# Performance work log

Hardware: AMD Instinct MI355X
Metric: run time of the kernel (lower is better)

## Reference

```python
import jax, jax.numpy as jnp
import numpy as np

B, N, D = 32, 2048, 128
HALF = D // 2
DT = 0.01  # interval = [0.0, 0.01], euler solver -> single step of size 0.01


def setup_inputs() -> dict:
    key = jax.random.key(0)
    ks = jax.random.split(key, 10)
    x = jax.random.normal(ks[0], (B, N, D), dtype=jnp.float32)
    hz = jax.random.normal(ks[1], (B, N, D), dtype=jnp.float32)
    # row-normalized random adjacency so adj @ h stays O(1) (avoids tanh saturation)
    adj = jax.random.uniform(ks[2], (N, N), dtype=jnp.float32) / N
    W1 = jax.random.normal(ks[3], (D, D), dtype=jnp.float32) * 0.05
    W2 = jax.random.normal(ks[4], (D, D), dtype=jnp.float32) * 0.05
    Wa = jax.random.normal(ks[5], (2 * D, 2 * D), dtype=jnp.float32) * 0.05
    ba = jnp.zeros((2 * D,), dtype=jnp.float32)
    Wb = jax.random.normal(ks[6], (2 * D, D), dtype=jnp.float32) * 0.05
    bb = jnp.zeros((D,), dtype=jnp.float32)
    # nn.Parameter init is zeros in torch; randomize in [0,0.1] for a nontrivial baseline
    eps = jax.random.uniform(ks[7], (B, N, HALF), dtype=jnp.float32) * 0.1
    return {"x": x, "hz": hz, "adj": adj, "W1": W1, "W2": W2,
            "Wa": Wa, "ba": ba, "Wb": Wb, "bb": bb, "eps": eps}


def reference(x, hz, adj, W1, W2, Wa, ba, Wb, bb, eps):
    # MLP gating: Linear(2D,2D) -> ReLU -> Linear(2D,D) -> Tanh
    u = jnp.concatenate([x, hz], axis=-1)            # [B,N,2D]
    h = jnp.tanh(jax.nn.relu(u @ Wa + ba) @ Wb + bb)  # [B,N,D]

    def gnn_func(h, W):
        # f(t, h) = tanh(A @ h @ W)  (graph diffusion ODE func)
        return jnp.tanh(jnp.einsum('nm,bmd->bnd', adj, h) @ W)

    def euler_step(h, W):
        # odeint(euler, t=[0, 0.01]): one step y1 = y0 + dt * f(0, y0)
        return h + DT * gnn_func(h, W)

    eps_c = jnp.clip(eps, 0.0, 0.1)
    for _ in range(2):
        h_f = euler_step(h, W1)[..., :HALF]                      # [B,N,D/2]
        h = jnp.concatenate([h_f, h[..., HALF:]], axis=-1)       # [B,N,D]
        h_s = eps_c * euler_step(h, W2)[..., HALF:]              # [B,N,D/2]
        h = jnp.concatenate([h_f, h_s], axis=-1)                 # [B,N,D]
    return h
```

## Files before the change

kernel.cpp:

```cpp
#include <hip/hip_runtime.h>


typedef unsigned short u16;
typedef unsigned int   u32;
typedef unsigned long long u64;
typedef __attribute__((ext_vector_type(8))) short bf8;
typedef __attribute__((ext_vector_type(4))) float f4;

#define AS1 __attribute__((address_space(1)))
#define AS3 __attribute__((address_space(3)))

__device__ __forceinline__ void gl_lds16(const void* g, void* l) {
  __builtin_amdgcn_global_load_lds((const AS1 u32*)g, (AS3 u32*)l, 16, 0, 0);
}
__device__ __forceinline__ float bf2f(u16 v) {
  u32 u = ((u32)v) << 16; return __builtin_bit_cast(float, u);
}
__device__ __forceinline__ u16 f2bf(float f) {
  u32 u = __builtin_bit_cast(u32, f);
  return (u16)((u + 0x7fffu + ((u >> 16) & 1u)) >> 16);
}
__device__ __forceinline__ float ldf(const void* p, size_t i, u32 isf32) {
  return isf32 ? ((const float*)p)[i] : bf2f(((const u16*)p)[i]);
}

__device__ __forceinline__ void stage128x32(const u16* grow0, int stride, u16* lds,
                                            int wave, int lane) {
  int r0 = wave * 16 + (lane >> 2);
  int c0 = (lane & 3) * 8;
  gl_lds16(grow0 + (size_t)r0 * stride + c0, lds + wave * 512);
  gl_lds16(grow0 + (size_t)(64 + r0) * stride + c0, lds + 2048 + wave * 512);
}
__device__ __forceinline__ void stage64x32(const u16* grow0, int stride, u16* lds,
                                           int wave, int lane) {
  gl_lds16(grow0 + (size_t)(wave * 16 + (lane >> 2)) * stride + (lane & 3) * 8,
           lds + wave * 512);
}

__global__ void detect_dtype(const u16* __restrict__ x_raw, u32* __restrict__ flag) {
  __shared__ int s;
  int tid = threadIdx.x;
  if (tid == 0) s = 0;
  __syncthreads();
  int huge = 0;
#pragma unroll
  for (int j = 0; j < 16; ++j) {
    u16 v = x_raw[tid * 16 + j];
    u32 e = (v >> 7) & 0xFF;
    if (e >= 0xC0) huge = 1;
  }
  if (huge) atomicOr(&s, 1);
  __syncthreads();
  if (tid == 0) flag[0] = (u32)s;
}

__global__ void cvt_bf16(const void* __restrict__ in, u16* __restrict__ out,
                         long in_off, int n, const u32* __restrict__ flag) {
  u32 isf32 = flag[0];
  int gid = blockIdx.x * 256 + threadIdx.x;
  long i = in_off + (long)gid * 4;
  if (gid * 4 >= n) return;
  u16 o0, o1, o2, o3;
  if (isf32) {
    f4 v = *(const f4*)&((const float*)in)[i];
    o0 = f2bf(v[0]); o1 = f2bf(v[1]); o2 = f2bf(v[2]); o3 = f2bf(v[3]);
  } else {
    u64 v = *(const u64*)&((const u16*)in)[i];
    o0 = (u16)v; o1 = (u16)(v >> 16); o2 = (u16)(v >> 32); o3 = (u16)(v >> 48);
  }
  u64 pk = (u64)o0 | ((u64)o1 << 16) | ((u64)o2 << 32) | ((u64)o3 << 48);
  *(u64*)&out[(size_t)gid * 4] = pk;
}

__global__ void prep_weights(const void* __restrict__ Wa, const void* __restrict__ Wb,
                             const void* __restrict__ W1, const void* __restrict__ W2,
                             u16* __restrict__ WaT, u16* __restrict__ WbT,
                             u16* __restrict__ W1T, u16* __restrict__ W2T,
                             const u32* __restrict__ flag) {
  u32 isf32 = flag[0];
  int i = blockIdx.x * 256 + threadIdx.x;
  if (i < 65536) {
    int o = i >> 8, k = i & 255; WaT[o * 256 + k] = f2bf(ldf(Wa, (size_t)k * 256 + o, isf32));
  } else if (i < 98304) {
    int j = i - 65536; int o = j >> 8, k = j & 255;
    WbT[o * 256 + k] = f2bf(ldf(Wb, (size_t)k * 128 + o, isf32));
  } else if (i < 106496) {
    int j = i - 98304; int jj = j >> 7, k = j & 127;
    W1T[jj * 128 + k] = f2bf(ldf(W1, (size_t)k * 128 + jj, isf32));
  } else {
    int j = i - 106496; int jj = j >> 7, k = j & 127;
    W2T[jj * 128 + k] = f2bf(ldf(W2, (size_t)k * 128 + 64 + jj, isf32));
  }
}

__global__ __launch_bounds__(256, 2) void mlp_fused(const void* __restrict__ x,
                                                    const void* __restrict__ hz,
                                                    const u16* __restrict__ WaT,
                                                    const void* __restrict__ ba,
                                                    const u16* __restrict__ WbT,
                                                    const void* __restrict__ bb,
                                                    const u16* __restrict__ W1T,
                                                    u16* __restrict__ hT,
                                                    u16* __restrict__ hW,
                                                    const u32* __restrict__ flag) {
  __shared__ __align__(16) u16 Z[64 * 264];
  __shared__ __align__(16) u16 pool[10240];
  u16* lA = pool;
  u16* lB = pool + 2048;
  u16* hN = pool;
  u32 isf32 = flag[0];
  int tid = threadIdx.x, lane = tid & 63, wave = tid >> 6;
  int col = lane & 15, quad = lane >> 4;
  int r0 = blockIdx.x * 64;
  int b = r0 >> 11;

  f4 acc[4][4] = {};
  for (int kk = 0; kk < 8; ++kk) {
    int k0 = kk * 32;
    const void* src = (kk < 4) ? x : hz;
    int csrc = (kk < 4) ? k0 : (k0 - 128);
    __syncthreads();
    {
      int row = tid >> 2, c0 = (tid & 3) * 8;
      size_t g = (size_t)(r0 + row) * 128 + csrc + c0;
      uint4 pk;
      if (isf32) {
        f4 v0 = *(const f4*)&((const float*)src)[g];
        f4 v1 = *(const f4*)&((const float*)src)[g + 4];
        pk.x = (u32)f2bf(v0[0]) | ((u32)f2bf(v0[1]) << 16);
        pk.y = (u32)f2bf(v0[2]) | ((u32)f2bf(v0[3]) << 16);
        pk.z = (u32)f2bf(v1[0]) | ((u32)f2bf(v1[1]) << 16);
        pk.w = (u32)f2bf(v1[2]) | ((u32)f2bf(v1[3]) << 16);
      } else {
        pk = *(const uint4*)&((const u16*)src)[g];
      }
      *(uint4*)&lA[row * 32 + c0] = pk;
    }
    stage128x32(WaT + k0, 256, lB, wave, lane);
    stage128x32(WaT + (size_t)128 * 256 + k0, 256, lB + 4096, wave, lane);
    __syncthreads();
    bf8 af[4], bfr[4];
#pragma unroll
    for (int mi = 0; mi < 4; ++mi) af[mi] = *(const bf8*)&lA[(mi * 16 + col) * 32 + quad * 8];
#pragma unroll
    for (int nj = 0; nj < 4; ++nj) bfr[nj] = *(const bf8*)&lB[(wave * 64 + nj * 16 + col) * 32 + quad * 8];
#pragma unroll
    for (int mi = 0; mi < 4; ++mi)
#pragma unroll
      for (int nj = 0; nj < 4; ++nj)
        acc[mi][nj] = __builtin_amdgcn_mfma_f32_16x16x32_bf16(af[mi], bfr[nj], acc[mi][nj], 0, 0, 0);
  }
#pragma unroll
  for (int mi = 0; mi < 4; ++mi)
#pragma unroll
    for (int nj = 0; nj < 4; ++nj) {
      int o = wave * 64 + nj * 16 + col;
      float bav = ldf(ba, o, isf32);
      int rl = mi * 16 + quad * 4;
#pragma unroll
      for (int r = 0; r < 4; ++r)
        Z[(rl + r) * 264 + o] = f2bf(fmaxf(acc[mi][nj][r] + bav, 0.f));
    }
  __syncthreads();

  f4 acc2[4][2] = {};
  for (int kk = 0; kk < 8; ++kk) {
    int k0 = kk * 32;
    if (kk) __syncthreads();
    stage128x32(WbT + k0, 256, lB, wave, lane);
    __syncthreads();
    bf8 az[4], bw[2];
#pragma unroll
    for (int mi = 0; mi < 4; ++mi) az[mi] = *(const bf8*)&Z[(mi * 16 + col) * 264 + k0 + quad * 8];
#pragma unroll
    for (int nj = 0; nj < 2; ++nj) bw[nj] = *(const bf8*)&lB[(wave * 32 + nj * 16 + col) * 32 + quad * 8];
#pragma unroll
    for (int mi = 0; mi < 4; ++mi)
#pragma unroll
      for (int nj = 0; nj < 2; ++nj)
        acc2[mi][nj] = __builtin_amdgcn_mfma_f32_16x16x32_bf16(az[mi], bw[nj], acc2[mi][nj], 0, 0, 0);
  }
  __syncthreads();

#pragma unroll
  for (int mi = 0; mi < 4; ++mi)
#pragma unroll
    for (int nj = 0; nj < 2; ++nj) {
      int d = wave * 32 + nj * 16 + col;
      float bbv = ldf(bb, d, isf32);
      int rl = mi * 16 + quad * 4;
      int rabs = r0 + rl;
      int n = rabs & 2047;
      u16 p[4];
#pragma unroll
      for (int r = 0; r < 4; ++r) {
        p[r] = f2bf(tanhf(acc2[mi][nj][r] + bbv));
        hN[(rl + r) * 136 + d] = p[r];
      }
      u64 pk = (u64)p[0] | ((u64)p[1] << 16) | ((u64)p[2] << 32) | ((u64)p[3] << 48);
      *(u64*)&hT[(size_t)(b * 128 + d) * 2048 + n] = pk;
    }
  __syncthreads();

  f4 acc3[4] = {};
#pragma unroll
  for (int ks = 0; ks < 4; ++ks) {
    bf8 aw[4], bg;
#pragma unroll
    for (int mi = 0; mi < 4; ++mi)
      aw[mi] = *(const bf8*)&W1T[(size_t)(mi * 16 + col) * 128 + ks * 32 + quad * 8];
    bg = *(const bf8*)&hN[(wave * 16 + col) * 136 + ks * 32 + quad * 8];
#pragma unroll
    for (int mi = 0; mi < 4; ++mi)
      acc3[mi] = __builtin_amdgcn_mfma_f32_16x16x32_bf16(aw[mi], bg, acc3[mi], 0, 0, 0);
  }
#pragma unroll
  for (int mi = 0; mi < 4; ++mi) {
    int rloc = wave * 16 + col;
    int ng = (r0 & 2047) + rloc;
#pragma unroll
    for (int r = 0; r < 4; ++r) {
      int j = mi * 16 + quad * 4 + r;
      hW[(size_t)(b * 64 + j) * 2048 + ng] = f2bf(acc3[mi][r]);
    }
  }
}

__global__ __launch_bounds__(256, 2) void fused_step2(const u16* __restrict__ hin,
                                                      const u16* __restrict__ hWT,
                                                      const u16* __restrict__ adjb,
                                                      const u16* __restrict__ WnT,
                                                      const void* __restrict__ eps,
                                                      u16* __restrict__ hout,
                                                      u16* __restrict__ hWout,
                                                      int half, const u32* __restrict__ flag) {
  __shared__ __align__(16) u16 smem[24576];
  u16* lA = smem;
  u16* lB = smem + 8192;
  u16* gN = smem;
  u32 isf32 = flag[0];
  int tid = threadIdx.x, lane = tid & 63, wave = tid >> 6;
  int col = lane & 15, quad = lane >> 4;
  int b = blockIdx.y;
  int n0 = blockIdx.x * 128;

  const u16* Arow = hWT + (size_t)(b * 64) * 2048;
  const u16* Brow = adjb + (size_t)n0 * 2048;

  f4 acc[4][2] = {};
  for (int kk = 0; kk < 16; ++kk) {
    int k0 = kk * 128;
#pragma unroll
    for (int p = 0; p < 4; ++p) {
      stage64x32(Arow + k0 + p * 32, 2048, lA + p * 2048, wave, lane);
      stage128x32(Brow + k0 + p * 32, 2048, lB + p * 4096, wave, lane);
    }
    __syncthreads();
#pragma unroll
    for (int p = 0; p < 4; ++p) {
      bf8 af[4], bfr[2];
#pragma unroll
      for (int mi = 0; mi < 4; ++mi) af[mi] = *(const bf8*)&lA[p * 2048 + (mi * 16 + col) * 32 + quad * 8];
#pragma unroll
      for (int nj = 0; nj < 2; ++nj) bfr[nj] = *(const bf8*)&lB[p * 4096 + (wave * 32 + nj * 16 + col) * 32 + quad * 8];
#pragma unroll
      for (int mi = 0; mi < 4; ++mi)
#pragma unroll
        for (int nj = 0; nj < 2; ++nj)
          acc[mi][nj] = __builtin_amdgcn_mfma_f32_16x16x32_bf16(af[mi], bfr[nj], acc[mi][nj], 0, 0, 0);
    }
    __syncthreads();
  }

  bool has_eps = (eps != nullptr);
  bool mk_hw = (WnT != nullptr);
  int dBase = half * 64;
#pragma unroll
  for (int mi = 0; mi < 4; ++mi)
#pragma unroll
    for (int nj = 0; nj < 2; ++nj) {
      int j0 = mi * 16 + quad * 4;
      int nl = wave * 32 + nj * 16 + col;
      int n = n0 + nl;
      float ev[4];
      if (has_eps) {
        size_t eoff = ((size_t)b * 2048 + n) * 64 + j0;
        if (isf32) {
          f4 e = *(const f4*)&((const float*)eps)[eoff];
          ev[0] = e[0]; ev[1] = e[1]; ev[2] = e[2]; ev[3] = e[3];
        } else {
          u64 e = *(const u64*)&((const u16*)eps)[eoff];
          ev[0] = bf2f((u16)e); ev[1] = bf2f((u16)(e >> 16));
          ev[2] = bf2f((u16)(e >> 32)); ev[3] = bf2f((u16)(e >> 48));
        }
      }
      u16 pv[4];
#pragma unroll
      for (int r = 0; r < 4; ++r) {
        int j = j0 + r;
        size_t idx = (size_t)(b * 128 + dBase + j) * 2048 + n;
        float hold = bf2f(hin[idx]);
        float nh = hold + 0.01f * tanhf(acc[mi][nj][r]);
        if (has_eps) {
          float e = fminf(fmaxf(ev[r], 0.f), 0.1f);
          nh = e * nh;
        }
        pv[r] = f2bf(nh);
        hout[idx] = pv[r];
      }
      if (mk_hw) {
        u64 pk = (u64)pv[0] | ((u64)pv[1] << 16) | ((u64)pv[2] << 32) | ((u64)pv[3] << 48);
        *(u64*)&gN[nl * 136 + dBase + j0] = pk;
      }
    }

  {
    int oh = (1 - half) * 64;
    const u16* src = hin + (size_t)(b * 128 + oh) * 2048 + n0;
    u16* dst = hout + (size_t)(b * 128 + oh) * 2048 + n0;
#pragma unroll
    for (int i = 0; i < 4; ++i) {
      int idx = i * 256 + tid;
      int rr = idx >> 4;
      int cc = (idx & 15) * 8;
      uint4 v = *(const uint4*)&src[(size_t)rr * 2048 + cc];
      *(uint4*)&dst[(size_t)rr * 2048 + cc] = v;
      if (mk_hw) {
        u16 t[8];
        *(uint4*)t = v;
#pragma unroll
        for (int q = 0; q < 8; ++q) gN[(cc + q) * 136 + oh + rr] = t[q];
      }
    }
  }

  if (mk_hw) {
    __syncthreads();
    f4 acc2[4][2] = {};
#pragma unroll
    for (int ks = 0; ks < 4; ++ks) {
      bf8 aw[4], bg[2];
#pragma unroll
      for (int mi = 0; mi < 4; ++mi)
        aw[mi] = *(const bf8*)&WnT[(size_t)(mi * 16 + col) * 128 + ks * 32 + quad * 8];
#pragma unroll
      for (int nj = 0; nj < 2; ++nj)
        bg[nj] = *(const bf8*)&gN[(wave * 32 + nj * 16 + col) * 136 + ks * 32 + quad * 8];
#pragma unroll
      for (int mi = 0; mi < 4; ++mi)
#pragma unroll
        for (int nj = 0; nj < 2; ++nj)
          acc2[mi][nj] = __builtin_amdgcn_mfma_f32_16x16x32_bf16(aw[mi], bg[nj], acc2[mi][nj], 0, 0, 0);
    }
#pragma unroll
    for (int mi = 0; mi < 4; ++mi)
#pragma unroll
      for (int nj = 0; nj < 2; ++nj) {
        int jp0 = mi * 16 + quad * 4;
        int n = n0 + wave * 32 + nj * 16 + col;
#pragma unroll
        for (int r = 0; r < 4; ++r)
          hWout[(size_t)(b * 64 + jp0 + r) * 2048 + n] = f2bf(acc2[mi][nj][r]);
      }
  }
}

__global__ void untranspose(const u16* __restrict__ hT, void* __restrict__ out,
                            const u32* __restrict__ flag) {
  __shared__ __align__(16) u16 t[64][65];
  u32 isf32 = flag[0];
  int b = blockIdx.z, d0 = blockIdx.y * 64, n0 = blockIdx.x * 64;
  int tid = threadIdx.x;
#pragma unroll
  for (int i = 0; i < 16; ++i) {
    int idx = tid + i * 256;
    int r = idx >> 6, c = idx & 63;
    t[r][c] = hT[(size_t)(b * 128 + d0 + r) * 2048 + n0 + c];
  }
  __syncthreads();
#pragma unroll
  for (int i = 0; i < 16; ++i) {
    int idx = tid + i * 256;
    int r = idx >> 6, c = idx & 63;
    size_t o = (size_t)(b * 2048 + n0 + r) * 128 + d0 + c;
    if (isf32) ((float*)out)[o] = bf2f(t[c][r]);
    else       ((u16*)out)[o] = t[c][r];
  }
}

extern "C" void kernel_launch(void* const* d_in, const int* in_sizes, int n_in,
                              void* d_out, int out_size, void* d_ws, size_t ws_size,
                              hipStream_t stream) {
  const void* x   = d_in[0];
  const void* hz  = d_in[1];
  const void* adj = d_in[2];
  const void* W1  = d_in[3];
  const void* W2  = d_in[4];
  const void* Wa  = d_in[5];
  const void* ba  = d_in[6];
  const void* Wb  = d_in[7];
  const void* bb  = d_in[8];
  const void* eps = d_in[9];

  char* ws = (char*)d_ws;
  u16* hA   = (u16*)(ws);
  u16* adjb = (u16*)(ws + (17ull << 20));
  u16* hWa  = (u16*)(ws + (26ull << 20));
  u16* hWb  = (u16*)(ws + (35ull << 20));
  u16* WaT  = (u16*)(ws + (44ull << 20));
  u16* WbT  = WaT + 256 * 256;
  u16* W1T  = WbT + 128 * 256;
  u16* W2T  = W1T + 64 * 128;
  u32* flag = (u32*)(W2T + 64 * 128);
  u16* hB   = (u16*)d_out;

  detect_dtype<<<dim3(1), dim3(256), 0, stream>>>((const u16*)x, flag);
  prep_weights<<<dim3(448), dim3(256), 0, stream>>>(Wa, Wb, W1, W2, WaT, WbT, W1T, W2T, flag);
  cvt_bf16<<<dim3(4096), dim3(256), 0, stream>>>(adj, adjb, 0, 4194304, flag);
  mlp_fused<<<dim3(1024), dim3(256), 0, stream>>>(x, hz, WaT, ba, WbT, bb, W1T, hA, hWa, flag);
  fused_step2<<<dim3(16, 32), dim3(256), 0, stream>>>(hA, hWa, adjb, W2T, nullptr, hB, hWb, 0, flag);
  fused_step2<<<dim3(16, 32), dim3(256), 0, stream>>>(hB, hWb, adjb, W1T, eps, hA, hWa, 1, flag);
  fused_step2<<<dim3(16, 32), dim3(256), 0, stream>>>(hA, hWa, adjb, W2T, nullptr, hB, hWb, 0, flag);
  fused_step2<<<dim3(16, 32), dim3(256), 0, stream>>>(hB, hWb, adjb, nullptr, eps, hA, nullptr, 1, flag);
  untranspose<<<dim3(32, 2, 32), dim3(256), 0, stream>>>(hA, d_out, flag);
}
```

Baseline: 350.1 us.

## Replace LDS staging with direct global register loads and register prefetch pipeline

Removes the LDS staging via global_load_lds in both the MLP kernel and the adjacency GEMM kernel. MFMA operands are now loaded straight from global memory into registers. The adjacency GEMM gains a 4-deep register ring buffer that prefetches three k-steps ahead with no __syncthreads. The MLP kernel drops its staging pool and raises its occupancy hint to 3 blocks per CU. In exchange, operand data is no longer shared across waves through LDS: each wave redundantly fetches its own A and B fragments through L1/L2 with narrow strided 16-byte loads, which may raise cache traffic.

```diff
diff --git a/kernel.cpp b/kernel.cpp
--- a/kernel.cpp
+++ b/kernel.cpp
@@ -7,12 +7,6 @@
 typedef __attribute__((ext_vector_type(8))) short bf8;
 typedef __attribute__((ext_vector_type(4))) float f4;
 
-#define AS1 __attribute__((address_space(1)))
-#define AS3 __attribute__((address_space(3)))
-
-__device__ __forceinline__ void gl_lds16(const void* g, void* l) {
-  __builtin_amdgcn_global_load_lds((const AS1 u32*)g, (AS3 u32*)l, 16, 0, 0);
-}
 __device__ __forceinline__ float bf2f(u16 v) {
   u32 u = ((u32)v) << 16; return __builtin_bit_cast(float, u);
 }
@@ -22,19 +16,6 @@
 }
 __device__ __forceinline__ float ldf(const void* p, size_t i, u32 isf32) {
   return isf32 ? ((const float*)p)[i] : bf2f(((const u16*)p)[i]);
-}
-
-__device__ __forceinline__ void stage128x32(const u16* grow0, int stride, u16* lds,
-                                            int wave, int lane) {
-  int r0 = wave * 16 + (lane >> 2);
-  int c0 = (lane & 3) * 8;
-  gl_lds16(grow0 + (size_t)r0 * stride + c0, lds + wave * 512);
-  gl_lds16(grow0 + (size_t)(64 + r0) * stride + c0, lds + 2048 + wave * 512);
-}
-__device__ __forceinline__ void stage64x32(const u16* grow0, int stride, u16* lds,
-                                           int wave, int lane) {
-  gl_lds16(grow0 + (size_t)(wave * 16 + (lane >> 2)) * stride + (lane & 3) * 8,
-           lds + wave * 512);
 }
 
 __global__ void detect_dtype(const u16* __restrict__ x_raw, u32* __restrict__ flag) {
@@ -93,7 +74,7 @@
   }
 }
 
-__global__ __launch_bounds__(256, 2) void mlp_fused(const void* __restrict__ x,
+__global__ __launch_bounds__(256, 3) void mlp_fused(const void* __restrict__ x,
                                                     const void* __restrict__ hz,
                                                     const u16* __restrict__ WaT,
                                                     const void* __restrict__ ba,
@@ -104,10 +85,7 @@
                                                     u16* __restrict__ hW,
                                                     const u32* __restrict__ flag) {
   __shared__ __align__(16) u16 Z[64 * 264];
-  __shared__ __align__(16) u16 pool[10240];
-  u16* lA = pool;
-  u16* lB = pool + 2048;
-  u16* hN = pool;
+  u16* hN = Z;
   u32 isf32 = flag[0];
   int tid = threadIdx.x, lane = tid & 63, wave = tid >> 6;
   int col = lane & 15, quad = lane >> 4;
@@ -115,35 +93,36 @@
   int b = r0 >> 11;
 
   f4 acc[4][4] = {};
+#pragma unroll 2
   for (int kk = 0; kk < 8; ++kk) {
     int k0 = kk * 32;
     const void* src = (kk < 4) ? x : hz;
     int csrc = (kk < 4) ? k0 : (k0 - 128);
-    __syncthreads();
-    {
-      int row = tid >> 2, c0 = (tid & 3) * 8;
-      size_t g = (size_t)(r0 + row) * 128 + csrc + c0;
-      uint4 pk;
-      if (isf32) {
+    bf8 af[4];
+    if (isf32) {
+#pragma unroll
+      for (int mi = 0; mi < 4; ++mi) {
+        size_t g = (size_t)(r0 + mi * 16 + col) * 128 + csrc + quad * 8;
         f4 v0 = *(const f4*)&((const float*)src)[g];
         f4 v1 = *(const f4*)&((const float*)src)[g + 4];
-        pk.x = (u32)f2bf(v0[0]) | ((u32)f2bf(v0[1]) << 16);
-        pk.y = (u32)f2bf(v0[2]) | ((u32)f2bf(v0[3]) << 16);
-        pk.z = (u32)f2bf(v1[0]) | ((u32)f2bf(v1[1]) << 16);
-        pk.w = (u32)f2bf(v1[2]) | ((u32)f2bf(v1[3]) << 16);
-      } else {
-        pk = *(const uint4*)&((const u16*)src)[g];
-      }
-      *(uint4*)&lA[row * 32 + c0] = pk;
-    }
-    stage128x32(WaT + k0, 256, lB, wave, lane);
-    stage128x32(WaT + (size_t)128 * 256 + k0, 256, lB + 4096, wave, lane);
-    __syncthreads();
-    bf8 af[4], bfr[4];
-#pragma unroll
-    for (int mi = 0; mi < 4; ++mi) af[mi] = *(const bf8*)&lA[(mi * 16 + col) * 32 + quad * 8];
-#pragma unroll
-    for (int nj = 0; nj < 4; ++nj) bfr[nj] = *(const bf8*)&lB[(wave * 64 + nj * 16 + col) * 32 + quad * 8];
+        bf8 t;
+        t[0] = (short)f2bf(v0[0]); t[1] = (short)f2bf(v0[1]);
+        t[2] = (short)f2bf(v0[2]); t[3] = (short)f2bf(v0[3]);
+        t[4] = (short)f2bf(v1[0]); t[5] = (short)f2bf(v1[1]);
+        t[6] = (short)f2bf(v1[2]); t[7] = (short)f2bf(v1[3]);
+        af[mi] = t;
+      }
+    } else {
+#pragma unroll
+      for (int mi = 0; mi < 4; ++mi) {
+        size_t g = (size_t)(r0 + mi * 16 + col) * 128 + csrc + quad * 8;
+        af[mi] = *(const bf8*)&((const u16*)src)[g];
+      }
+    }
+    bf8 bfr[4];
+#pragma unroll
+    for (int nj = 0; nj < 4; ++nj)
+      bfr[nj] = *(const bf8*)&WaT[(size_t)(wave * 64 + nj * 16 + col) * 256 + k0 + quad * 8];
 #pragma unroll
     for (int mi = 0; mi < 4; ++mi)
 #pragma unroll
@@ -164,16 +143,15 @@
   __syncthreads();
 
   f4 acc2[4][2] = {};
+#pragma unroll 2
   for (int kk = 0; kk < 8; ++kk) {
     int k0 = kk * 32;
-    if (kk) __syncthreads();
-    stage128x32(WbT + k0, 256, lB, wave, lane);
-    __syncthreads();
     bf8 az[4], bw[2];
 #pragma unroll
     for (int mi = 0; mi < 4; ++mi) az[mi] = *(const bf8*)&Z[(mi * 16 + col) * 264 + k0 + quad * 8];
 #pragma unroll
-    for (int nj = 0; nj < 2; ++nj) bw[nj] = *(const bf8*)&lB[(wave * 32 + nj * 16 + col) * 32 + quad * 8];
+    for (int nj = 0; nj < 2; ++nj)
+      bw[nj] = *(const bf8*)&WbT[(size_t)(wave * 32 + nj * 16 + col) * 256 + k0 + quad * 8];
 #pragma unroll
     for (int mi = 0; mi < 4; ++mi)
 #pragma unroll
@@ -189,8 +167,7 @@
       int d = wave * 32 + nj * 16 + col;
       float bbv = ldf(bb, d, isf32);
       int rl = mi * 16 + quad * 4;
-      int rabs = r0 + rl;
-      int n = rabs & 2047;
+      int n = (r0 + rl) & 2047;
       u16 p[4];
 #pragma unroll
       for (int r = 0; r < 4; ++r) {
@@ -216,8 +193,7 @@
   }
 #pragma unroll
   for (int mi = 0; mi < 4; ++mi) {
-    int rloc = wave * 16 + col;
-    int ng = (r0 & 2047) + rloc;
+    int ng = (r0 & 2047) + wave * 16 + col;
 #pragma unroll
     for (int r = 0; r < 4; ++r) {
       int j = mi * 16 + quad * 4 + r;
@@ -234,42 +210,48 @@
                                                       u16* __restrict__ hout,
                                                       u16* __restrict__ hWout,
                                                       int half, const u32* __restrict__ flag) {
-  __shared__ __align__(16) u16 smem[24576];
-  u16* lA = smem;
-  u16* lB = smem + 8192;
-  u16* gN = smem;
+  __shared__ __align__(16) u16 gN[128 * 136];
   u32 isf32 = flag[0];
   int tid = threadIdx.x, lane = tid & 63, wave = tid >> 6;
   int col = lane & 15, quad = lane >> 4;
   int b = blockIdx.y;
   int n0 = blockIdx.x * 128;
 
-  const u16* Arow = hWT + (size_t)(b * 64) * 2048;
-  const u16* Brow = adjb + (size_t)n0 * 2048;
+  const u16* aRow[4];
+  const u16* bRow[2];
+#pragma unroll
+  for (int mi = 0; mi < 4; ++mi)
+    aRow[mi] = hWT + (size_t)(b * 64 + mi * 16 + col) * 2048 + quad * 8;
+#pragma unroll
+  for (int nj = 0; nj < 2; ++nj)
+    bRow[nj] = adjb + (size_t)(n0 + wave * 32 + nj * 16 + col) * 2048 + quad * 8;
+
+  bf8 aP[4][4], bP[4][2];
+#pragma unroll
+  for (int s = 0; s < 3; ++s) {
+#pragma unroll
+    for (int mi = 0; mi < 4; ++mi) aP[s][mi] = *(const bf8*)(aRow[mi] + s * 32);
+#pragma unroll
+    for (int nj = 0; nj < 2; ++nj) bP[s][nj] = *(const bf8*)(bRow[nj] + s * 32);
+  }
 
   f4 acc[4][2] = {};
-  for (int kk = 0; kk < 16; ++kk) {
-    int k0 = kk * 128;
-#pragma unroll
-    for (int p = 0; p < 4; ++p) {
-      stage64x32(Arow + k0 + p * 32, 2048, lA + p * 2048, wave, lane);
-      stage128x32(Brow + k0 + p * 32, 2048, lB + p * 4096, wave, lane);
-    }
-    __syncthreads();
-#pragma unroll
-    for (int p = 0; p < 4; ++p) {
-      bf8 af[4], bfr[2];
-#pragma unroll
-      for (int mi = 0; mi < 4; ++mi) af[mi] = *(const bf8*)&lA[p * 2048 + (mi * 16 + col) * 32 + quad * 8];
-#pragma unroll
-      for (int nj = 0; nj < 2; ++nj) bfr[nj] = *(const bf8*)&lB[p * 4096 + (wave * 32 + nj * 16 + col) * 32 + quad * 8];
-#pragma unroll
-      for (int mi = 0; mi < 4; ++mi)
-#pragma unroll
-        for (int nj = 0; nj < 2; ++nj)
-          acc[mi][nj] = __builtin_amdgcn_mfma_f32_16x16x32_bf16(af[mi], bfr[nj], acc[mi][nj], 0, 0, 0);
-    }
-    __syncthreads();
+#pragma unroll 4
+  for (int kk = 0; kk < 64; ++kk) {
+    int cur = kk & 3;
+    if (kk < 61) {
+      int nx = (kk + 3) & 3;
+      int ko = (kk + 3) * 32;
+#pragma unroll
+      for (int mi = 0; mi < 4; ++mi) aP[nx][mi] = *(const bf8*)(aRow[mi] + ko);
+#pragma unroll
+      for (int nj = 0; nj < 2; ++nj) bP[nx][nj] = *(const bf8*)(bRow[nj] + ko);
+    }
+#pragma unroll
+    for (int mi = 0; mi < 4; ++mi)
+#pragma unroll
+      for (int nj = 0; nj < 2; ++nj)
+        acc[mi][nj] = __builtin_amdgcn_mfma_f32_16x16x32_bf16(aP[cur][mi], bP[cur][nj], acc[mi][nj], 0, 0, 0);
   }
 
   bool has_eps = (eps != nullptr);
```

Result: slower. 628.9 us (+79.7%).

## Split MLP into two kernels and halve fused_step2 tile for occupancy

Applied to the files above, without the earlier changes.

The fused MLP kernel is split into mlp1, which writes the ReLU hidden layer Z1 (B*N x 256 bf16) to global memory in 128x128 tiles, and mlp2, which reloads it for the second linear, tanh and W1 projection. Dropping the big per-block Z tile in LDS allows a launch bound of 4 blocks per CU. fused_step2 now uses 64-node tiles with half the LDS and four blocks per CU, doubling the grid. The cost is an extra global round-trip of Z1 (staged in the output buffer) and less reuse of hW loads per adjacency tile in fused_step2.

```diff
diff --git a/kernel.cpp b/kernel.cpp
--- a/kernel.cpp
+++ b/kernel.cpp
@@ -93,26 +93,19 @@
   }
 }
 
-__global__ __launch_bounds__(256, 2) void mlp_fused(const void* __restrict__ x,
-                                                    const void* __restrict__ hz,
-                                                    const u16* __restrict__ WaT,
-                                                    const void* __restrict__ ba,
-                                                    const u16* __restrict__ WbT,
-                                                    const void* __restrict__ bb,
-                                                    const u16* __restrict__ W1T,
-                                                    u16* __restrict__ hT,
-                                                    u16* __restrict__ hW,
-                                                    const u32* __restrict__ flag) {
-  __shared__ __align__(16) u16 Z[64 * 264];
-  __shared__ __align__(16) u16 pool[10240];
-  u16* lA = pool;
-  u16* lB = pool + 2048;
-  u16* hN = pool;
+__global__ __launch_bounds__(256, 4) void mlp1(const void* __restrict__ x,
+                                               const void* __restrict__ hz,
+                                               const u16* __restrict__ WaT,
+                                               const void* __restrict__ ba,
+                                               u16* __restrict__ Z1,
+                                               const u32* __restrict__ flag) {
+  __shared__ __align__(16) u16 lA[128 * 32];
+  __shared__ __align__(16) u16 lB[128 * 32];
   u32 isf32 = flag[0];
   int tid = threadIdx.x, lane = tid & 63, wave = tid >> 6;
-  int col = lane & 15, quad = lane >> 4;
-  int r0 = blockIdx.x * 64;
-  int b = r0 >> 11;
+  int wm = wave >> 1, wn = wave & 1, col = lane & 15, quad = lane >> 4;
+  int r0g = blockIdx.y * 128;
+  int o0 = blockIdx.x * 128;
 
   f4 acc[4][4] = {};
   for (int kk = 0; kk < 8; ++kk) {
@@ -121,29 +114,38 @@
     int csrc = (kk < 4) ? k0 : (k0 - 128);
     __syncthreads();
     {
-      int row = tid >> 2, c0 = (tid & 3) * 8;
-      size_t g = (size_t)(r0 + row) * 128 + csrc + c0;
-      uint4 pk;
+      int row = tid >> 1, c0 = (tid & 1) * 16;
+      size_t g = (size_t)(r0g + row) * 128 + csrc + c0;
+      uint4 p0, p1;
       if (isf32) {
-        f4 v0 = *(const f4*)&((const float*)src)[g];
-        f4 v1 = *(const f4*)&((const float*)src)[g + 4];
-        pk.x = (u32)f2bf(v0[0]) | ((u32)f2bf(v0[1]) << 16);
-        pk.y = (u32)f2bf(v0[2]) | ((u32)f2bf(v0[3]) << 16);
-        pk.z = (u32)f2bf(v1[0]) | ((u32)f2bf(v1[1]) << 16);
-        pk.w = (u32)f2bf(v1[2]) | ((u32)f2bf(v1[3]) << 16);
+        const float* fp = (const float*)src + g;
+        f4 v0 = *(const f4*)(fp);
+        f4 v1 = *(const f4*)(fp + 4);
+        f4 v2 = *(const f4*)(fp + 8);
+        f4 v3 = *(const f4*)(fp + 12);
+        p0.x = (u32)f2bf(v0[0]) | ((u32)f2bf(v0[1]) << 16);
+        p0.y = (u32)f2bf(v0[2]) | ((u32)f2bf(v0[3]) << 16);
+        p0.z = (u32)f2bf(v1[0]) | ((u32)f2bf(v1[1]) << 16);
+        p0.w = (u32)f2bf(v1[2]) | ((u32)f2bf(v1[3]) << 16);
+        p1.x = (u32)f2bf(v2[0]) | ((u32)f2bf(v2[1]) << 16);
+        p1.y = (u32)f2bf(v2[2]) | ((u32)f2bf(v2[3]) << 16);
+        p1.z = (u32)f2bf(v3[0]) | ((u32)f2bf(v3[1]) << 16);
+        p1.w = (u32)f2bf(v3[2]) | ((u32)f2bf(v3[3]) << 16);
       } else {
-        pk = *(const uint4*)&((const u16*)src)[g];
-      }
-      *(uint4*)&lA[row * 32 + c0] = pk;
-    }
-    stage128x32(WaT + k0, 256, lB, wave, lane);
-    stage128x32(WaT + (size_t)128 * 256 + k0, 256, lB + 4096, wave, lane);
+        const u16* up = (const u16*)src + g;
+        p0 = *(const uint4*)(up);
+        p1 = *(const uint4*)(up + 8);
+      }
+      *(uint4*)&lA[row * 32 + c0] = p0;
+      *(uint4*)&lA[row * 32 + c0 + 8] = p1;
+    }
+    stage128x32(WaT + (size_t)o0 * 256 + k0, 256, lB, wave, lane);
     __syncthreads();
     bf8 af[4], bfr[4];
 #pragma unroll
-    for (int mi = 0; mi < 4; ++mi) af[mi] = *(const bf8*)&lA[(mi * 16 + col) * 32 + quad * 8];
-#pragma unroll
-    for (int nj = 0; nj < 4; ++nj) bfr[nj] = *(const bf8*)&lB[(wave * 64 + nj * 16 + col) * 32 + quad * 8];
+    for (int mi = 0; mi < 4; ++mi) af[mi] = *(const bf8*)&lA[(wm * 64 + mi * 16 + col) * 32 + quad * 8];
+#pragma unroll
+    for (int nj = 0; nj < 4; ++nj) bfr[nj] = *(const bf8*)&lB[(wn * 64 + nj * 16 + col) * 32 + quad * 8];
 #pragma unroll
     for (int mi = 0; mi < 4; ++mi)
 #pragma unroll
@@ -154,31 +156,49 @@
   for (int mi = 0; mi < 4; ++mi)
 #pragma unroll
     for (int nj = 0; nj < 4; ++nj) {
-      int o = wave * 64 + nj * 16 + col;
+      int o = o0 + wn * 64 + nj * 16 + col;
       float bav = ldf(ba, o, isf32);
-      int rl = mi * 16 + quad * 4;
+      int rb = r0g + wm * 64 + mi * 16 + quad * 4;
 #pragma unroll
       for (int r = 0; r < 4; ++r)
-        Z[(rl + r) * 264 + o] = f2bf(fmaxf(acc[mi][nj][r] + bav, 0.f));
-    }
-  __syncthreads();
-
-  f4 acc2[4][2] = {};
+        Z1[(size_t)(rb + r) * 256 + o] = f2bf(fmaxf(acc[mi][nj][r] + bav, 0.f));
+    }
+}
+
+__global__ __launch_bounds__(256, 4) void mlp2(const u16* __restrict__ Z1,
+                                               const u16* __restrict__ WbT,
+                                               const void* __restrict__ bb,
+                                               const u16* __restrict__ W1T,
+                                               u16* __restrict__ hT,
+                                               u16* __restrict__ hW,
+                                               const u32* __restrict__ flag) {
+  __shared__ __align__(16) u16 pool[9216];
+  u16* lA = pool;
+  u16* lB = pool + 2048;
+  u16* hN = pool;
+  u32 isf32 = flag[0];
+  int tid = threadIdx.x, lane = tid & 63, wave = tid >> 6;
+  int col = lane & 15, quad = lane >> 4;
+  int r0 = blockIdx.x * 64;
+  int b = r0 >> 11;
+
+  f4 acc[4][2] = {};
   for (int kk = 0; kk < 8; ++kk) {
     int k0 = kk * 32;
     if (kk) __syncthreads();
+    stage64x32(Z1 + (size_t)r0 * 256 + k0, 256, lA, wave, lane);
     stage128x32(WbT + k0, 256, lB, wave, lane);
     __syncthreads();
     bf8 az[4], bw[2];
 #pragma unroll
-    for (int mi = 0; mi < 4; ++mi) az[mi] = *(const bf8*)&Z[(mi * 16 + col) * 264 + k0 + quad * 8];
+    for (int mi = 0; mi < 4; ++mi) az[mi] = *(const bf8*)&lA[(mi * 16 + col) * 32 + quad * 8];
 #pragma unroll
     for (int nj = 0; nj < 2; ++nj) bw[nj] = *(const bf8*)&lB[(wave * 32 + nj * 16 + col) * 32 + quad * 8];
 #pragma unroll
     for (int mi = 0; mi < 4; ++mi)
 #pragma unroll
       for (int nj = 0; nj < 2; ++nj)
-        acc2[mi][nj] = __builtin_amdgcn_mfma_f32_16x16x32_bf16(az[mi], bw[nj], acc2[mi][nj], 0, 0, 0);
+        acc[mi][nj] = __builtin_amdgcn_mfma_f32_16x16x32_bf16(az[mi], bw[nj], acc[mi][nj], 0, 0, 0);
   }
   __syncthreads();
 
@@ -189,12 +209,11 @@
       int d = wave * 32 + nj * 16 + col;
       float bbv = ldf(bb, d, isf32);
       int rl = mi * 16 + quad * 4;
-      int rabs = r0 + rl;
-      int n = rabs & 2047;
+      int n = (r0 + rl) & 2047;
       u16 p[4];
 #pragma unroll
       for (int r = 0; r < 4; ++r) {
-        p[r] = f2bf(tanhf(acc2[mi][nj][r] + bbv));
+        p[r] = f2bf(tanhf(acc[mi][nj][r] + bbv));
         hN[(rl + r) * 136 + d] = p[r];
       }
       u64 pk = (u64)p[0] | ((u64)p[1] << 16) | ((u64)p[2] << 32) | ((u64)p[3] << 48);
@@ -216,8 +235,7 @@
   }
 #pragma unroll
   for (int mi = 0; mi < 4; ++mi) {
-    int rloc = wave * 16 + col;
-    int ng = (r0 & 2047) + rloc;
+    int ng = (r0 & 2047) + wave * 16 + col;
 #pragma unroll
     for (int r = 0; r < 4; ++r) {
       int j = mi * 16 + quad * 4 + r;
@@ -226,7 +244,7 @@
   }
 }
 
-__global__ __launch_bounds__(256, 2) void fused_step2(const u16* __restrict__ hin,
+__global__ __launch_bounds__(256, 4) void fused_step2(const u16* __restrict__ hin,
                                                       const u16* __restrict__ hWT,
                                                       const u16* __restrict__ adjb,
                                                       const u16* __restrict__ WnT,
@@ -234,7 +252,7 @@
                                                       u16* __restrict__ hout,
                                                       u16* __restrict__ hWout,
                                                       int half, const u32* __restrict__ flag) {
-  __shared__ __align__(16) u16 smem[24576];
+  __shared__ __align__(16) u16 smem[16384];
   u16* lA = smem;
   u16* lB = smem + 8192;
   u16* gN = smem;
@@ -242,87 +260,83 @@
   int tid = threadIdx.x, lane = tid & 63, wave = tid >> 6;
   int col = lane & 15, quad = lane >> 4;
   int b = blockIdx.y;
-  int n0 = blockIdx.x * 128;
+  int n0 = blockIdx.x * 64;
 
   const u16* Arow = hWT + (size_t)(b * 64) * 2048;
   const u16* Brow = adjb + (size_t)n0 * 2048;
 
-  f4 acc[4][2] = {};
+  f4 acc[4] = {};
   for (int kk = 0; kk < 16; ++kk) {
     int k0 = kk * 128;
+    if (kk) __syncthreads();
 #pragma unroll
     for (int p = 0; p < 4; ++p) {
       stage64x32(Arow + k0 + p * 32, 2048, lA + p * 2048, wave, lane);
-      stage128x32(Brow + k0 + p * 32, 2048, lB + p * 4096, wave, lane);
+      stage64x32(Brow + k0 + p * 32, 2048, lB + p * 2048, wave, lane);
     }
     __syncthreads();
 #pragma unroll
     for (int p = 0; p < 4; ++p) {
-      bf8 af[4], bfr[2];
+      bf8 af[4], bfr;
 #pragma unroll
       for (int mi = 0; mi < 4; ++mi) af[mi] = *(const bf8*)&lA[p * 2048 + (mi * 16 + col) * 32 + quad * 8];
-#pragma unroll
-      for (int nj = 0; nj < 2; ++nj) bfr[nj] = *(const bf8*)&lB[p * 4096 + (wave * 32 + nj * 16 + col) * 32 + quad * 8];
+      bfr = *(const bf8*)&lB[p * 2048 + (wave * 16 + col) * 32 + quad * 8];
 #pragma unroll
       for (int mi = 0; mi < 4; ++mi)
-#pragma unroll
-        for (int nj = 0; nj < 2; ++nj)
-          acc[mi][nj] = __builtin_amdgcn_mfma_f32_16x16x32_bf16(af[mi], bfr[nj], acc[mi][nj], 0, 0, 0);
-    }
-    __syncthreads();
-  }
+        acc[mi] = __builtin_amdgcn_mfma_f32_16x16x32_bf16(af[mi], bfr, acc[mi], 0, 0, 0);
+    }
+  }
+  __syncthreads();
 
   bool has_eps = (eps != nullptr);
   bool mk_hw = (WnT != nullptr);
   int dBase = half * 64;
 #pragma unroll
-  for (int mi = 0; mi < 4; ++mi)
-#pragma unroll
-    for (int nj = 0; nj < 2; ++nj) {
-      int j0 = mi * 16 + quad * 4;
-      int nl = wave * 32 + nj * 16 + col;
-      int n = n0 + nl;
-      float ev[4];
+  for (int mi = 0; mi < 4; ++mi) {
+    int j0 = mi * 16 + quad * 4;
+    int nl = wave * 16 + col;
+    int n = n0 + nl;
+    float ev[4];
+    if (has_eps) {
+      size_t eoff = ((size_t)b * 2048 + n) * 64 + j0;
+      if (isf32) {
+        f4 e = *(const f4*)&((const float*)eps)[eoff];
+        ev[0] = e[0]; ev[1] = e[1]; ev[2] = e[2]; ev[3] = e[3];
+      } else {
+        u64 e = *(const u64*)&((const u16*)eps)[eoff];
+        ev[0] = bf2f((u16)e); ev[1] = bf2f((u16)(e >> 16));
+        ev[2] = bf2f((u16)(e >> 32)); ev[3] = bf2f((u16)(e >> 48));
+      }
+    }
+    u16 pv[4];
+#pragma unroll
+    for (int r = 0; r < 4; ++r) {
+      int j = j0 + r;
+      size_t idx = (size_t)(b * 128 + dBase + j) * 2048 + n;
+      float hold = bf2f(hin[idx]);
+      float nh = hold + 0.01f * tanhf(acc[mi][r]);
       if (has_eps) {
-        size_t eoff = ((size_t)b * 2048 + n) * 64 + j0;
-        if (isf32) {
-          f4 e = *(const f4*)&((const float*)eps)[eoff];
-          ev[0] = e[0]; ev[1] = e[1]; ev[2] = e[2]; ev[3] = e[3];
-        } else {
-          u64 e = *(const u64*)&((const u16*)eps)[eoff];
-          ev[0] = bf2f((u16)e); ev[1] = bf2f((u16)(e >> 16));
-          ev[2] = bf2f((u16)(e >> 32)); ev[3] = bf2f((u16)(e >> 48));
-        }
-      }
-      u16 pv[4];
-#pragma unroll
-      for (int r = 0; r < 4; ++r) {
-        int j = j0 + r;
-        size_t idx = (size_t)(b * 128 + dBase + j) * 2048 + n;
-        float hold = bf2f(hin[idx]);
-        float nh = hold + 0.01f * tanhf(acc[mi][nj][r]);
-        if (has_eps) {
-          float e = fminf(fmaxf(ev[r], 0.f), 0.1f);
-          nh = e * nh;
-        }
-        pv[r] = f2bf(nh);
-        hout[idx] = pv[r];
-      }
-      if (mk_hw) {
-        u64 pk = (u64)pv[0] | ((u64)pv[1] << 16) | ((u64)pv[2] << 32) | ((u64)pv[3] << 48);
-        *(u64*)&gN[nl * 136 + dBase + j0] = pk;
-      }
-    }
+        float e = fminf(fmaxf(ev[r], 0.f), 0.1f);
+        nh = e * nh;
+      }
+      pv[r] = f2bf(nh);
+      hout[idx] = pv[r];
+    }
+    if (mk_hw) {
+      u64 pk = (u64)pv[0] | ((u64)pv[1] << 16) | ((u64)pv[2] << 32) | ((u64)pv[3] << 48);
+      *(u64*)&gN[nl * 136 + dBase + j0] = pk;
+    }
+  }
 
   {
     int oh = (1 - half) * 64;
     const u16* src = hin + (size_t)(b * 128 + oh) * 2048 + n0;
     u16* dst = hout + (size_t)(b * 128 + oh) * 2048 + n0;
 #pragma unroll
-    for (int i = 0; i < 4; ++i) {
+    for (int i = 0; i < 2; ++i) {
       int idx = i * 256 + tid;
-      int rr = idx >> 4;
-      int cc = (idx & 15) * 8;
+      int rr = idx >> 3;
+      int cc = (idx & 7) * 8;
       uint4 v = *(const uint4*)&src[(size_t)rr * 2048 + cc];
       *(uint4*)&dst[(size_t)rr * 2048 + cc] = v;
       if (mk_hw) {
@@ -336,32 +350,27 @@
 
   if (mk_hw) {
     __syncthreads();
-    f4 acc2[4][2] = {};
+    f4 acc2[4] = {};
 #pragma unroll
     for (int ks = 0; ks < 4; ++ks) {
-      bf8 aw[4], bg[2];
+      bf8 aw[4], bg;
 #pragma unroll
       for (int mi = 0; mi < 4; ++mi)
         aw[mi] = *(const bf8*)&WnT[(size_t)(mi * 16 + col) * 128 + ks * 32 + quad * 8];
-#pragma unroll
-      for (int nj = 0; nj < 2; ++nj)
-        bg[nj] = *(const bf8*)&gN[(wave * 32 + nj * 16 + col) * 136 + ks * 32 + quad * 8];
+      bg = *(const bf8*)&gN[(wave * 16 + col) * 136 + ks * 32 + quad * 8];
 #pragma unroll
       for (int mi = 0; mi < 4; ++mi)
-#pragma unroll
-        for (int nj = 0; nj < 2; ++nj)
-          acc2[mi][nj] = __builtin_amdgcn_mfma_f32_16x16x32_bf16(aw[mi], bg[nj], acc2[mi][nj], 0, 0, 0);
-    }
-#pragma unroll
-    for (int mi = 0; mi < 4; ++mi)
-#pragma unroll
-      for (int nj = 0; nj < 2; ++nj) {
-        int jp0 = mi * 16 + quad * 4;
-        int n = n0 + wave * 32 + nj * 16 + col;
-#pragma unroll
-        for (int r = 0; r < 4; ++r)
-          hWout[(size_t)(b * 64 + jp0 + r) * 2048 + n] = f2bf(acc2[mi][nj][r]);
-      }
+        acc2[mi] = __builtin_amdgcn_mfma_f32_16x16x32_bf16(aw[mi], bg, acc2[mi], 0, 0, 0);
+    }
+#pragma unroll
+    for (int mi = 0; mi < 4; ++mi) {
+      int n = n0 + wave * 16 + col;
+#pragma unroll
+      for (int r = 0; r < 4; ++r) {
+        int jp = mi * 16 + quad * 4 + r;
+        hWout[(size_t)(b * 64 + jp) * 2048 + n] = f2bf(acc2[mi][r]);
+      }
+    }
   }
 }
 
@@ -412,15 +421,17 @@
   u16* W1T  = WbT + 128 * 256;
   u16* W2T  = W1T + 64 * 128;
   u32* flag = (u32*)(W2T + 64 * 128);
+  u16* Z1   = (u16*)d_out;
   u16* hB   = (u16*)d_out;
 
   detect_dtype<<<dim3(1), dim3(256), 0, stream>>>((const u16*)x, flag);
   prep_weights<<<dim3(448), dim3(256), 0, stream>>>(Wa, Wb, W1, W2, WaT, WbT, W1T, W2T, flag);
   cvt_bf16<<<dim3(4096), dim3(256), 0, stream>>>(adj, adjb, 0, 4194304, flag);
-  mlp_fused<<<dim3(1024), dim3(256), 0, stream>>>(x, hz, WaT, ba, WbT, bb, W1T, hA, hWa, flag);
-  fused_step2<<<dim3(16, 32), dim3(256), 0, stream>>>(hA, hWa, adjb, W2T, nullptr, hB, hWb, 0, flag);
-  fused_step2<<<dim3(16, 32), dim3(256), 0, stream>>>(hB, hWb, adjb, W1T, eps, hA, hWa, 1, flag);
-  fused_step2<<<dim3(16, 32), dim3(256), 0, stream>>>(hA, hWa, adjb, W2T, nullptr, hB, hWb, 0, flag);
-  fused_step2<<<dim3(16, 32), dim3(256), 0, stream>>>(hB, hWb, adjb, nullptr, eps, hA, nullptr, 1, flag);
+  mlp1<<<dim3(2, 512), dim3(256), 0, stream>>>(x, hz, WaT, ba, Z1, flag);
+  mlp2<<<dim3(1024), dim3(256), 0, stream>>>(Z1, WbT, bb, W1T, hA, hWa, flag);
+  fused_step2<<<dim3(32, 32), dim3(256), 0, stream>>>(hA, hWa, adjb, W2T, nullptr, hB, hWb, 0, flag);
+  fused_step2<<<dim3(32, 32), dim3(256), 0, stream>>>(hB, hWb, adjb, W1T, eps, hA, hWa, 1, flag);
+  fused_step2<<<dim3(32, 32), dim3(256), 0, stream>>>(hA, hWa, adjb, W2T, nullptr, hB, hWb, 0, flag);
+  fused_step2<<<dim3(32, 32), dim3(256), 0, stream>>>(hB, hWb, adjb, nullptr, eps, hA, nullptr, 1, flag);
   untranspose<<<dim3(32, 2, 32), dim3(256), 0, stream>>>(hA, d_out, flag);
 }
```

Result: slower. 380.7 us (+8.8%).
